# Performance work log

Measured on AMD Instinct MI355X. Metric: run time of the kernel, lower is better.

The kernel has to match this reference:

```python
import jax, jax.numpy as jnp
import numpy as np

B, C, H, W, TF, NH = 16, 512, 24, 24, 512, 8
CPH = C // NH  # channels per head = 64


def setup_inputs() -> dict:
    key = jax.random.key(0)
    ks = jax.random.split(key, 10)
    s = 0.02
    return {
        "x": jax.random.normal(ks[0], (B, C, H, W), jnp.float32),
        "t": jax.random.normal(ks[1], (B, TF), jnp.float32),
        "Wk": jax.random.normal(ks[2], (C, C), jnp.float32) * s,      # 1x1 conv, no bias
        "Wq": jax.random.normal(ks[3], (C, C), jnp.float32) * s,      # 1x1 conv, no bias
        "Wt_w": jax.random.normal(ks[4], (C, TF), jnp.float32) * s,   # Linear weight (out,in)
        "Wt_b": jnp.zeros((C,), jnp.float32),
        "Wm": jax.random.normal(ks[5], (C, C + TF), jnp.float32) * s, # merge 1x1 conv, no bias
        "Wv": jax.random.normal(ks[6], (C, C), jnp.float32) * s,      # 1x1 conv, no bias
        "Wr_w": jax.random.normal(ks[7], (C, C), jnp.float32) * s,    # 1x1 conv with bias
        "Wr_b": jnp.zeros((C,), jnp.float32),
    }


def reference(x, t, Wk, Wq, Wt_w, Wt_b, Wm, Wv, Wr_w, Wr_b):
    b, c, h, w = x.shape
    hw = h * w
    scale = 1.0 / np.sqrt(CPH).astype(np.float32)

    # broadcast text features spatially and merge with image features (1x1 conv)
    t_r = jnp.broadcast_to(t[:, :, None, None], (b, t.shape[1], h, w))
    vl = jnp.einsum('oc,bchw->bohw', Wm, jnp.concatenate([x, t_r], axis=1))
    values = jnp.einsum('oc,bchw->bohw', Wv, vl).reshape(b, NH, CPH, hw)

    # self-attention map: softmax over keys (last dim)
    keys = jnp.einsum('oc,bchw->bohw', Wk, x).reshape(b, NH, CPH, hw)
    queries = jnp.einsum('oc,bchw->bohw', Wq, x).reshape(b, NH, CPH, hw)
    self_att = jax.nn.softmax(
        jnp.einsum('bhcn,bhcm->bhnm', queries, keys) * scale, axis=-1)

    # global cross-attention map: text query vs spatial positions, softmax over hw
    t_m = (t @ Wt_w.T + Wt_b).reshape(b, NH, CPH)
    cross = jax.nn.softmax(
        jnp.einsum('bhcm,bhc->bhm', x.reshape(b, NH, CPH, hw), t_m) * scale, axis=-1)

    # additive combination, then value-weighted aggregation
    att = self_att + cross[:, :, None, :]                    # [b, nh, hw_q, hw_k]
    out = jnp.einsum('bhcm,bhnm->bhcn', values, att).reshape(b, c, h, w)
    out = jnp.einsum('oc,bchw->bohw', Wr_w, out) + Wr_b[None, :, None, None]
    return out
```

## Files before the change

### kernel.cpp

```cpp
#include <hip/hip_runtime.h>
#include <cstdint>
#include <cstddef>

#define NB    16
#define NC    512
#define NHW   576
#define NTF   512
#define NHEAD 8
#define NCPH  64
#define ATT_SCALE 0.125f
#define SCALE_L2E 0.18033688011112042f

typedef float  floatx4 __attribute__((ext_vector_type(4)));
typedef short  short8  __attribute__((ext_vector_type(8)));
typedef unsigned short ushortx4 __attribute__((ext_vector_type(4)));

__device__ __forceinline__ unsigned short f2bf(float f) {
    unsigned int u = __float_as_uint(f);
    u += 0x7fffu + ((u >> 16) & 1u);
    return (unsigned short)(u >> 16);
}
__device__ __forceinline__ float bf2f(unsigned short h) {
    return __uint_as_float(((unsigned int)h) << 16);
}


__global__ void k_prep_weights(const float* __restrict__ Wq, const float* __restrict__ Wk,
                               const float* __restrict__ Wv, const float* __restrict__ Wr,
                               unsigned short* __restrict__ Wqkm,
                               unsigned short* __restrict__ Wv_bf,
                               unsigned short* __restrict__ Wr_bf) {
    int i = blockIdx.x * 256 + threadIdx.x;
    if (i < 1024 * 512) {
        int r = i >> 9, c = i & 511;
        float v = (r < 512) ? Wq[r * 512 + c] : Wk[(r - 512) * 512 + c];
        Wqkm[i] = f2bf(v);
    } else {
        int j = i - 1024 * 512;
        if (j < 512 * 512) Wv_bf[j] = f2bf(Wv[j]);
        else               Wr_bf[j - 512 * 512] = f2bf(Wr[j - 512 * 512]);
    }
}

__global__ void k_prep_wmT(const float* __restrict__ Wm, unsigned short* __restrict__ WmT) {
    __shared__ float tile[32][33];
    int n0 = blockIdx.x * 32, k0 = blockIdx.y * 32;
    int tx = threadIdx.x, ty = threadIdx.y;
    #pragma unroll
    for (int k = 0; k < 4; k++)
        tile[ty + k * 8][tx] = Wm[(size_t)(k0 + ty + k * 8) * 1024 + n0 + tx];
    __syncthreads();
    #pragma unroll
    for (int k = 0; k < 4; k++)
        WmT[(size_t)(n0 + ty + k * 8) * 512 + k0 + tx] = f2bf(tile[tx][ty + k * 8]);
}

__global__ void k_prep_xT(const float* __restrict__ x, unsigned short* __restrict__ xT) {
    __shared__ float tile[32][33];
    int b  = blockIdx.z;
    int p0 = blockIdx.x * 32, c0 = blockIdx.y * 32;
    int tx = threadIdx.x, ty = threadIdx.y;
    const float* xb = x + (size_t)b * NC * NHW;
    #pragma unroll
    for (int k = 0; k < 4; k++)
        tile[ty + k * 8][tx] = xb[(size_t)(c0 + ty + k * 8) * NHW + p0 + tx];
    __syncthreads();
    unsigned short* xTb = xT + (size_t)b * NHW * NC;
    #pragma unroll
    for (int k = 0; k < 4; k++)
        xTb[(size_t)(p0 + ty + k * 8) * NC + c0 + tx] = f2bf(tile[tx][ty + k * 8]);
}

__global__ void k_prep_t(const float* __restrict__ t, const float* __restrict__ Wt_w,
                         const float* __restrict__ Wt_b, const float* __restrict__ Wvm_txt,
                         float* __restrict__ tm, float* __restrict__ tmerge) {
    __shared__ float ts[512];
    int b = blockIdx.x;
    int tid = threadIdx.x;
    ts[tid]       = t[b * 512 + tid];
    ts[tid + 256] = t[b * 512 + tid + 256];
    __syncthreads();
    int oo = blockIdx.y * 256 + tid;
    const float* Wrow = (oo < 512) ? (Wt_w + (size_t)oo * 512)
                                   : (Wvm_txt + (size_t)(oo - 512) * 512);
    float acc = 0.f;
    #pragma unroll 4
    for (int c = 0; c < 512; c += 4) {
        float4 w = *reinterpret_cast<const float4*>(Wrow + c);
        acc += w.x * ts[c] + w.y * ts[c + 1] + w.z * ts[c + 2] + w.w * ts[c + 3];
    }
    if (oo < 512) tm[b * 512 + oo] = acc + Wt_b[oo];
    else          tmerge[b * 512 + (oo - 512)] = acc;
}


__device__ __forceinline__ void g128_stage(const unsigned short* __restrict__ src,
                                           unsigned short* lds, int tid) {
    int row  = tid >> 3;
    int slot = (tid & 7) ^ (row & 7);
    #pragma unroll
    for (int i = 0; i < 4; i++) {
        __builtin_amdgcn_global_load_lds(
            (const __attribute__((address_space(1))) unsigned int*)(src + (size_t)(32 * i + row) * NC + slot * 8),
            (__attribute__((address_space(3))) unsigned int*)(lds + i * 2048 + tid * 8), 16, 0, 0);
    }
}

__device__ __forceinline__ void g128_main(const unsigned short* __restrict__ Asrc,
                                          const unsigned short* __restrict__ Bsrc,
                                          unsigned short (*At)[8192], unsigned short (*Bt)[8192],
                                          int tid, int lane, int wr, int wc,
                                          floatx4 (&acc)[4][4]) {
    int cl = lane & 15, hi = lane >> 4, sx = cl & 7;

    g128_stage(Asrc, At[0], tid);
    g128_stage(Bsrc, Bt[0], tid);
    __syncthreads();

    int buf = 0;
    for (int ks = 0; ks < 8; ks++) {
        if (ks < 7) {
            g128_stage(Asrc + (ks + 1) * 64, At[buf ^ 1], tid);
            g128_stage(Bsrc + (ks + 1) * 64, Bt[buf ^ 1], tid);
        }
        #pragma unroll
        for (int kk = 0; kk < 2; kk++) {
            int sl = ((kk << 2) + hi) ^ sx;
            short8 a[4], bb[4];
            #pragma unroll
            for (int i = 0; i < 4; i++)
                a[i] = *reinterpret_cast<const short8*>(&At[buf][(wr * 64 + i * 16 + cl) * 64 + sl * 8]);
            #pragma unroll
            for (int j = 0; j < 4; j++)
                bb[j] = *reinterpret_cast<const short8*>(&Bt[buf][(wc * 64 + j * 16 + cl) * 64 + sl * 8]);
            #pragma unroll
            for (int i = 0; i < 4; i++)
                #pragma unroll
                for (int j = 0; j < 4; j++)
                    acc[i][j] = __builtin_amdgcn_mfma_f32_16x16x32_bf16(a[i], bb[j], acc[i][j], 0, 0, 0);
        }
        __syncthreads();
        buf ^= 1;
    }
}

__global__ void k_fold(const unsigned short* __restrict__ Wv_bf,
                       const unsigned short* __restrict__ WmT,
                       unsigned short* __restrict__ Wqkm,
                       float* __restrict__ Wvm_txt) {
    __shared__ unsigned short At[2][8192], Bt[2][8192];
    int tid = threadIdx.x, lane = tid & 63, wid = tid >> 6;
    int wr = wid >> 1, wc = wid & 1;
    int m = blockIdx.x >> 3, nt = blockIdx.x & 7;
    int o0 = m * 128, n0 = nt * 128;

    floatx4 acc[4][4];
    floatx4 zz = {0.f, 0.f, 0.f, 0.f};
    #pragma unroll
    for (int i = 0; i < 4; i++)
        #pragma unroll
        for (int j = 0; j < 4; j++) acc[i][j] = zz;

    g128_main(Wv_bf + (size_t)o0 * NC, WmT + (size_t)n0 * NC, At, Bt, tid, lane, wr, wc, acc);

    int cl = lane & 15, r0 = (lane >> 4) * 4;
    #pragma unroll
    for (int i = 0; i < 4; i++)
        #pragma unroll
        for (int jn = 0; jn < 4; jn++) {
            int n = n0 + wc * 64 + jn * 16 + cl;
            #pragma unroll
            for (int j = 0; j < 4; j++) {
                int o = o0 + wr * 64 + i * 16 + r0 + j;
                if (n0 < 512) Wqkm[(size_t)(1024 + o) * 512 + n] = f2bf(acc[i][jn][j]);
                else          Wvm_txt[(size_t)o * 512 + (n - 512)] = acc[i][jn][j];
            }
        }
}

__global__ void k_gemm_qkm(const unsigned short* __restrict__ Wqkm,
                           const unsigned short* __restrict__ xT,
                           const float* __restrict__ tmerge,
                           unsigned short* __restrict__ QT,
                           unsigned short* __restrict__ KT,
                           unsigned short* __restrict__ V) {
    __shared__ unsigned short At[2][8192], Bt[2][8192];
    int tid = threadIdx.x, lane = tid & 63, wid = tid >> 6;
    int wr = wid >> 1, wc = wid & 1;
    int bid = blockIdx.x;
    int xcd = bid & 7, slot = bid >> 3;
    int m = slot / 9, nl = slot % 9;
    int n0 = (xcd * 9 + nl) * 128;
    int o0 = m * 128;

    floatx4 acc[4][4];
    floatx4 zz = {0.f, 0.f, 0.f, 0.f};
    #pragma unroll
    for (int i = 0; i < 4; i++)
        #pragma unroll
        for (int j = 0; j < 4; j++) acc[i][j] = zz;

    g128_main(Wqkm + (size_t)o0 * NC, xT + (size_t)n0 * NC, At, Bt, tid, lane, wr, wc, acc);

    int cl = lane & 15, r0 = (lane >> 4) * 4;
    int ob = (m & 3) * 128 + wr * 64;

    if (m < 8) {
        unsigned short* Yt = (m < 4) ? QT : KT;
        #pragma unroll
        for (int i = 0; i < 4; i++) {
            int ol = ob + i * 16 + r0;
            #pragma unroll
            for (int jn = 0; jn < 4; jn++) {
                int n = n0 + wc * 64 + jn * 16 + cl;
                ushortx4 pk;
                pk[0] = f2bf(acc[i][jn][0]);
                pk[1] = f2bf(acc[i][jn][1]);
                pk[2] = f2bf(acc[i][jn][2]);
                pk[3] = f2bf(acc[i][jn][3]);
                *reinterpret_cast<ushortx4*>(Yt + (size_t)n * NC + ol) = pk;
            }
        }
    } else {
        #pragma unroll
        for (int i = 0; i < 4; i++) {
            int ol = ob + i * 16 + r0;
            #pragma unroll
            for (int jn = 0; jn < 4; jn++) {
                int n = n0 + wc * 64 + jn * 16 + cl;
                int b = n / NHW, p = n - b * NHW;
                float4 tv = *reinterpret_cast<const float4*>(tmerge + b * NC + ol);
                float bias[4] = {tv.x, tv.y, tv.z, tv.w};
                #pragma unroll
                for (int j = 0; j < 4; j++)
                    V[((size_t)b * NC + ol + j) * NHW + p] = f2bf(acc[i][jn][j] + bias[j]);
            }
        }
    }
}

__global__ void k_gemm_final(const unsigned short* __restrict__ Wr_bf,
                             const unsigned short* __restrict__ AO,
                             const float* __restrict__ Wr_b,
                             float* __restrict__ out) {
    __shared__ unsigned short At[2][8192], Bt[2][8192];
    int tid = threadIdx.x, lane = tid & 63, wid = tid >> 6;
    int wr = wid >> 1, wc = wid & 1;
    int bid = blockIdx.x;
    int xcd = bid & 7, slot = bid >> 3;
    int m = slot / 9, nl = slot % 9;
    int n0 = (xcd * 9 + nl) * 128;
    int o0 = m * 128;

    floatx4 acc[4][4];
    floatx4 zz = {0.f, 0.f, 0.f, 0.f};
    #pragma unroll
    for (int i = 0; i < 4; i++)
        #pragma unroll
        for (int j = 0; j < 4; j++) acc[i][j] = zz;

    g128_main(Wr_bf + (size_t)o0 * NC, AO + (size_t)n0 * NC, At, Bt, tid, lane, wr, wc, acc);

    int cl = lane & 15, r0 = (lane >> 4) * 4;
    #pragma unroll
    for (int i = 0; i < 4; i++) {
        float4 bv = *reinterpret_cast<const float4*>(Wr_b + o0 + wr * 64 + i * 16 + r0);
        float bias[4] = {bv.x, bv.y, bv.z, bv.w};
        #pragma unroll
        for (int jn = 0; jn < 4; jn++) {
            int n = n0 + wc * 64 + jn * 16 + cl;
            int b = n / NHW, p = n - b * NHW;
            #pragma unroll
            for (int j = 0; j < 4; j++) {
                int c = o0 + wr * 64 + i * 16 + r0 + j;
                out[((size_t)b * NC + c) * NHW + p] = acc[i][jn][j] + bias[j];
            }
        }
    }
}


__global__ void k_cross_o2(const unsigned short* __restrict__ xT,
                           const unsigned short* __restrict__ V,
                           const float* __restrict__ tm,
                           float* __restrict__ o2) {
    __shared__ float tms[64];
    __shared__ float ss[576];
    __shared__ float red[8];
    __shared__ float part[4][64];
    int bh = blockIdx.x;
    int b = bh >> 3, h = bh & 7;
    int tid = threadIdx.x;

    if (tid < 64) tms[tid] = tm[b * 512 + h * 64 + tid];
    __syncthreads();

    for (int m = tid; m < 576; m += 256) {
        const short8* xr8 = reinterpret_cast<const short8*>(xT + ((size_t)b * NHW + m) * NC + h * 64);
        float acc = 0.f;
        #pragma unroll
        for (int cc = 0; cc < 8; cc++) {
            short8 v8 = xr8[cc];
            #pragma unroll
            for (int q = 0; q < 8; q++)
                acc += bf2f((unsigned short)v8[q]) * tms[cc * 8 + q];
        }
        ss[m] = acc * ATT_SCALE;
    }
    __syncthreads();

    float pmax = -3e38f;
    for (int m = tid; m < 576; m += 256) pmax = fmaxf(pmax, ss[m]);
    #pragma unroll
    for (int off = 32; off; off >>= 1) pmax = fmaxf(pmax, __shfl_xor(pmax, off));
    if ((tid & 63) == 0) red[tid >> 6] = pmax;
    __syncthreads();
    float mx = fmaxf(fmaxf(red[0], red[1]), fmaxf(red[2], red[3]));

    float psum = 0.f;
    for (int m = tid; m < 576; m += 256) {
        float e = __expf(ss[m] - mx);
        ss[m] = e;
        psum += e;
    }
    #pragma unroll
    for (int off = 32; off; off >>= 1) psum += __shfl_xor(psum, off);
    if ((tid & 63) == 0) red[4 + (tid >> 6)] = psum;
    __syncthreads();
    float inv = 1.f / (red[4] + red[5] + red[6] + red[7]);

    int c = tid & 63, seg = tid >> 6;
    const unsigned short* vr = V + ((size_t)b * NC + h * 64 + c) * NHW;
    float pa = 0.f;
    for (int m = seg * 144; m < seg * 144 + 144; m++) pa += bf2f(vr[m]) * ss[m];
    part[seg][c] = pa;
    __syncthreads();
    if (tid < 64)
        o2[(b * 8 + h) * 64 + tid] =
            (part[0][tid] + part[1][tid] + part[2][tid] + part[3][tid]) * inv;
}


__global__ void k_attn(const unsigned short* __restrict__ QT,
                       const unsigned short* __restrict__ KT,
                       const unsigned short* __restrict__ V,
                       const float* __restrict__ o2,
                       unsigned short* __restrict__ AO) {
    __shared__ unsigned short Ktile[2][64][64];
    __shared__ unsigned short Vtile[2][64][64];
    __shared__ unsigned short pbuf[4][16][88];
    int tid  = threadIdx.x;
    int lane = tid & 63, wid = tid >> 6;

    int bid  = blockIdx.x;
    int xcd  = bid & 7;
    int slot = bid >> 3;
    int bh   = xcd * 16 + slot / 9;
    int qt   = slot % 9;
    int b = bh >> 3, h = bh & 7;
    int n0 = qt * 64 + wid * 16;
    int cl = lane & 15;
    int r0 = (lane >> 4) * 4;
    int part = lane >> 4;
    int ko = part * 8;

    const unsigned short* Qb = QT + ((size_t)b * NHW + n0) * NC + h * 64;
    const unsigned short* Kb = KT + (size_t)b * NHW * NC + h * 64;
    const unsigned short* Vb = V  + ((size_t)b * NC + h * 64) * NHW;

    short8 aq0 = *reinterpret_cast<const short8*>(Qb + (size_t)cl * NC + ko);
    short8 aq1 = *reinterpret_cast<const short8*>(Qb + (size_t)cl * NC + 32 + ko);

    int srow = lane >> 3;
    int scol = (lane & 7) ^ srow;

    floatx4 zz = {0.f, 0.f, 0.f, 0.f};
    floatx4 oacc[4] = {zz, zz, zz, zz};
    float es[4] = {0.f, 0.f, 0.f, 0.f};

    {
        const unsigned short* ks = Kb + (size_t)(wid * 16 + srow) * NC + scol * 8;
        const unsigned short* vs = Vb + (size_t)(wid * 16 + srow) * NHW + scol * 8;
        #pragma unroll
        for (int i = 0; i < 2; i++) {
            __builtin_amdgcn_global_load_lds(
                (const __attribute__((address_space(1))) unsigned int*)(ks + (size_t)i * 8 * NC),
                (__attribute__((address_space(3))) unsigned int*)&Ktile[0][wid * 16 + i * 8][0], 16, 0, 0);
            __builtin_amdgcn_global_load_lds(
                (const __attribute__((address_space(1))) unsigned int*)(vs + (size_t)i * 8 * NHW),
                (__attribute__((address_space(3))) unsigned int*)&Vtile[0][wid * 16 + i * 8][0], 16, 0, 0);
        }
    }
    __syncthreads();

    int buf = 0;
    for (int chk = 0; chk < 9; chk++) {
        int m0 = chk * 64;
        if (chk < 8) {
            const unsigned short* ks = Kb + (size_t)(m0 + 64 + wid * 16 + srow) * NC + scol * 8;
            const unsigned short* vs = Vb + (size_t)(wid * 16 + srow) * NHW + (m0 + 64) + scol * 8;
            #pragma unroll
            for (int i = 0; i < 2; i++) {
                __builtin_amdgcn_global_load_lds(
                    (const __attribute__((address_space(1))) unsigned int*)(ks + (size_t)i * 8 * NC),
                    (__attribute__((address_space(3))) unsigned int*)&Ktile[buf ^ 1][wid * 16 + i * 8][0], 16, 0, 0);
                __builtin_amdgcn_global_load_lds(
                    (const __attribute__((address_space(1))) unsigned int*)(vs + (size_t)i * 8 * NHW),
                    (__attribute__((address_space(3))) unsigned int*)&Vtile[buf ^ 1][wid * 16 + i * 8][0], 16, 0, 0);
            }
        }

        floatx4 s[4];
        #pragma unroll
        for (int t = 0; t < 4; t++) {
            int row = t * 16 + cl;
            int sw = cl & 7;
            short8 bk0 = *reinterpret_cast<const short8*>(&Ktile[buf][row][(part ^ sw) * 8]);
            short8 bk1 = *reinterpret_cast<const short8*>(&Ktile[buf][row][((part + 4) ^ sw) * 8]);
            s[t] = __builtin_amdgcn_mfma_f32_16x16x32_bf16(aq0, bk0, zz, 0, 0, 0);
            s[t] = __builtin_amdgcn_mfma_f32_16x16x32_bf16(aq1, bk1, s[t], 0, 0, 0);
        }
        #pragma unroll
        for (int t = 0; t < 4; t++)
            #pragma unroll
            for (int j = 0; j < 4; j++) {
                float e = exp2f(s[t][j] * SCALE_L2E);
                es[j] += e;
                pbuf[wid][r0 + j][t * 16 + cl] = f2bf(e);
            }
        short8 pa0 = *reinterpret_cast<const short8*>(&pbuf[wid][cl][ko]);
        short8 pa1 = *reinterpret_cast<const short8*>(&pbuf[wid][cl][32 + ko]);
        #pragma unroll
        for (int ct = 0; ct < 4; ct++) {
            int row = ct * 16 + cl;
            int sw = cl & 7;
            short8 bv0 = *reinterpret_cast<const short8*>(&Vtile[buf][row][(part ^ sw) * 8]);
            short8 bv1 = *reinterpret_cast<const short8*>(&Vtile[buf][row][((part + 4) ^ sw) * 8]);
            oacc[ct] = __builtin_amdgcn_mfma_f32_16x16x32_bf16(pa0, bv0, oacc[ct], 0, 0, 0);
            oacc[ct] = __builtin_amdgcn_mfma_f32_16x16x32_bf16(pa1, bv1, oacc[ct], 0, 0, 0);
        }
        __syncthreads();
        buf ^= 1;
    }

    #pragma unroll
    for (int off = 1; off < 16; off <<= 1)
        #pragma unroll
        for (int j = 0; j < 4; j++) es[j] += __shfl_xor(es[j], off);
    float ri[4];
    #pragma unroll
    for (int j = 0; j < 4; j++) ri[j] = 1.f / es[j];

    const float* o2b = o2 + bh * 64;
    #pragma unroll
    for (int ct = 0; ct < 4; ct++) {
        float o2v = o2b[ct * 16 + cl];
        #pragma unroll
        for (int j = 0; j < 4; j++)
            pbuf[wid][r0 + j][ct * 16 + cl] = f2bf(oacc[ct][j] * ri[j] + o2v);
    }
    short8 w0 = *reinterpret_cast<const short8*>(&pbuf[wid][cl][part * 16]);
    short8 w1 = *reinterpret_cast<const short8*>(&pbuf[wid][cl][part * 16 + 8]);
    unsigned short* dst = AO + ((size_t)b * NHW + n0 + cl) * NC + h * 64 + part * 16;
    *reinterpret_cast<short8*>(dst)     = w0;
    *reinterpret_cast<short8*>(dst + 8) = w1;
}


extern "C" void kernel_launch(void* const* d_in, const int* in_sizes, int n_in,
                              void* d_out, int out_size, void* d_ws, size_t ws_size,
                              hipStream_t stream) {
    const float* x    = (const float*)d_in[0];
    const float* t    = (const float*)d_in[1];
    const float* Wk   = (const float*)d_in[2];
    const float* Wq   = (const float*)d_in[3];
    const float* Wt_w = (const float*)d_in[4];
    const float* Wt_b = (const float*)d_in[5];
    const float* Wm   = (const float*)d_in[6];
    const float* Wv   = (const float*)d_in[7];
    const float* Wr_w = (const float*)d_in[8];
    const float* Wr_b = (const float*)d_in[9];
    float* out = (float*)d_out;
    char* ws = (char*)d_ws;

    unsigned short* xT      = (unsigned short*)(ws);
    unsigned short* Wqkm    = (unsigned short*)(ws + 9437184);
    unsigned short* Wv_bf   = (unsigned short*)(ws + 11010048);
    unsigned short* Wr_bf   = (unsigned short*)(ws + 11534336);
    float*          tm      = (float*)(ws + 12058624);
    float*          tmerge  = (float*)(ws + 12091392);
    unsigned short* QT      = (unsigned short*)(ws + 12124160);
    unsigned short* KT      = (unsigned short*)(ws + 21561344);
    unsigned short* WmT     = (unsigned short*)(ws + 30998528);
    float*          Wvm_txt = (float*)(ws + 32047104);
    unsigned short* Vv      = (unsigned short*)(ws + 40435712);
    float*          o2      = (float*)(ws + 49872896);
    unsigned short* AO      = xT;
    (void)in_sizes; (void)n_in; (void)out_size; (void)ws_size;

    k_prep_weights<<<4096, 256, 0, stream>>>(Wq, Wk, Wv, Wr_w, Wqkm, Wv_bf, Wr_bf);
    k_prep_wmT<<<dim3(32, 16), dim3(32, 8), 0, stream>>>(Wm, WmT);
    k_prep_xT<<<dim3(18, 16, 16), dim3(32, 8), 0, stream>>>(x, xT);
    k_fold<<<32, 256, 0, stream>>>(Wv_bf, WmT, Wqkm, Wvm_txt);
    k_prep_t<<<dim3(16, 4), 256, 0, stream>>>(t, Wt_w, Wt_b, Wvm_txt, tm, tmerge);
    k_gemm_qkm<<<864, 256, 0, stream>>>(Wqkm, xT, tmerge, QT, KT, Vv);
    k_cross_o2<<<128, 256, 0, stream>>>(xT, Vv, tm, o2);
    k_attn<<<1152, 256, 0, stream>>>(QT, KT, Vv, o2, AO);
    k_gemm_final<<<288, 256, 0, stream>>>(Wr_bf, AO, Wr_b, out);
}
```

Baseline: 124.4 us.

## Merge prep kernels and compute text merge term as matvecs instead of folded matrix

```diff
diff --git a/kernel.cpp b/kernel.cpp
--- a/kernel.cpp
+++ b/kernel.cpp
@@ -24,42 +24,50 @@
     return __uint_as_float(((unsigned int)h) << 16);
 }
 
-
-__global__ void k_prep_weights(const float* __restrict__ Wq, const float* __restrict__ Wk,
-                               const float* __restrict__ Wv, const float* __restrict__ Wr,
-                               unsigned short* __restrict__ Wqkm,
-                               unsigned short* __restrict__ Wv_bf,
-                               unsigned short* __restrict__ Wr_bf) {
-    int i = blockIdx.x * 256 + threadIdx.x;
-    if (i < 1024 * 512) {
-        int r = i >> 9, c = i & 511;
-        float v = (r < 512) ? Wq[r * 512 + c] : Wk[(r - 512) * 512 + c];
-        Wqkm[i] = f2bf(v);
-    } else {
-        int j = i - 1024 * 512;
-        if (j < 512 * 512) Wv_bf[j] = f2bf(Wv[j]);
-        else               Wr_bf[j - 512 * 512] = f2bf(Wr[j - 512 * 512]);
-    }
-}
-
-__global__ void k_prep_wmT(const float* __restrict__ Wm, unsigned short* __restrict__ WmT) {
+__global__ void k_prep_all(const float* __restrict__ Wq, const float* __restrict__ Wk,
+                           const float* __restrict__ Wv, const float* __restrict__ Wr,
+                           const float* __restrict__ Wm, const float* __restrict__ x,
+                           unsigned short* __restrict__ Wqkm,
+                           unsigned short* __restrict__ Wv_bf,
+                           unsigned short* __restrict__ Wr_bf,
+                           unsigned short* __restrict__ WmT,
+                           unsigned short* __restrict__ xT) {
     __shared__ float tile[32][33];
-    int n0 = blockIdx.x * 32, k0 = blockIdx.y * 32;
-    int tx = threadIdx.x, ty = threadIdx.y;
-    #pragma unroll
-    for (int k = 0; k < 4; k++)
-        tile[ty + k * 8][tx] = Wm[(size_t)(k0 + ty + k * 8) * 1024 + n0 + tx];
-    __syncthreads();
-    #pragma unroll
-    for (int k = 0; k < 4; k++)
-        WmT[(size_t)(n0 + ty + k * 8) * 512 + k0 + tx] = f2bf(tile[tx][ty + k * 8]);
-}
-
-__global__ void k_prep_xT(const float* __restrict__ x, unsigned short* __restrict__ xT) {
-    __shared__ float tile[32][33];
-    int b  = blockIdx.z;
-    int p0 = blockIdx.x * 32, c0 = blockIdx.y * 32;
-    int tx = threadIdx.x, ty = threadIdx.y;
+    int bid = blockIdx.x;
+    int tid = threadIdx.x;
+
+    if (bid < 4096) {
+        int i = bid * 256 + tid;
+        if (i < 1024 * 512) {
+            int r = i >> 9, c = i & 511;
+            float v = (r < 512) ? Wq[r * 512 + c] : Wk[(r - 512) * 512 + c];
+            Wqkm[i] = f2bf(v);
+        } else {
+            int j = i - 1024 * 512;
+            if (j < 512 * 512) Wv_bf[j] = f2bf(Wv[j]);
+            else               Wr_bf[j - 512 * 512] = f2bf(Wr[j - 512 * 512]);
+        }
+        return;
+    }
+
+    int tx = tid & 31, ty = tid >> 5;
+    if (bid < 4352) {
+        int bi = bid - 4096;
+        int n0 = (bi & 15) * 32, k0 = (bi >> 4) * 32;
+        #pragma unroll
+        for (int k = 0; k < 4; k++)
+            tile[ty + k * 8][tx] = Wm[(size_t)(k0 + ty + k * 8) * 1024 + n0 + tx];
+        __syncthreads();
+        #pragma unroll
+        for (int k = 0; k < 4; k++)
+            WmT[(size_t)(n0 + ty + k * 8) * 512 + k0 + tx] = f2bf(tile[tx][ty + k * 8]);
+        return;
+    }
+
+    int bi = bid - 4352;
+    int pi = bi % 18, rem = bi / 18;
+    int ci = rem & 15, b = rem >> 4;
+    int p0 = pi * 32, c0 = ci * 32;
     const float* xb = x + (size_t)b * NC * NHW;
     #pragma unroll
     for (int k = 0; k < 4; k++)
@@ -72,25 +80,50 @@
 }
 
 __global__ void k_prep_t(const float* __restrict__ t, const float* __restrict__ Wt_w,
-                         const float* __restrict__ Wt_b, const float* __restrict__ Wvm_txt,
+                         const float* __restrict__ Wt_b, const float* __restrict__ Wm,
+                         const float* __restrict__ Wv,
                          float* __restrict__ tm, float* __restrict__ tmerge) {
     __shared__ float ts[512];
-    int b = blockIdx.x;
-    int tid = threadIdx.x;
+    __shared__ float us[512];
+    int b = blockIdx.x, tid = threadIdx.x;
     ts[tid]       = t[b * 512 + tid];
     ts[tid + 256] = t[b * 512 + tid + 256];
     __syncthreads();
-    int oo = blockIdx.y * 256 + tid;
-    const float* Wrow = (oo < 512) ? (Wt_w + (size_t)oo * 512)
-                                   : (Wvm_txt + (size_t)(oo - 512) * 512);
-    float acc = 0.f;
-    #pragma unroll 4
-    for (int c = 0; c < 512; c += 4) {
-        float4 w = *reinterpret_cast<const float4*>(Wrow + c);
-        acc += w.x * ts[c] + w.y * ts[c + 1] + w.z * ts[c + 2] + w.w * ts[c + 3];
-    }
-    if (oo < 512) tm[b * 512 + oo] = acc + Wt_b[oo];
-    else          tmerge[b * 512 + (oo - 512)] = acc;
+
+    if (blockIdx.y == 0) {
+        for (int oo = tid; oo < 512; oo += 256) {
+            const float* Wrow = Wt_w + (size_t)oo * 512;
+            float acc = 0.f;
+            #pragma unroll 4
+            for (int c = 0; c < 512; c += 4) {
+                float4 w = *reinterpret_cast<const float4*>(Wrow + c);
+                acc += w.x * ts[c] + w.y * ts[c + 1] + w.z * ts[c + 2] + w.w * ts[c + 3];
+            }
+            tm[b * 512 + oo] = acc + Wt_b[oo];
+        }
+    } else {
+        for (int c = tid; c < 512; c += 256) {
+            const float* Wrow = Wm + (size_t)c * 1024 + 512;
+            float acc = 0.f;
+            #pragma unroll 4
+            for (int j = 0; j < 512; j += 4) {
+                float4 w = *reinterpret_cast<const float4*>(Wrow + j);
+                acc += w.x * ts[j] + w.y * ts[j + 1] + w.z * ts[j + 2] + w.w * ts[j + 3];
+            }
+            us[c] = acc;
+        }
+        __syncthreads();
+        for (int oo = tid; oo < 512; oo += 256) {
+            const float* Wrow = Wv + (size_t)oo * 512;
+            float acc = 0.f;
+            #pragma unroll 4
+            for (int c = 0; c < 512; c += 4) {
+                float4 w = *reinterpret_cast<const float4*>(Wrow + c);
+                acc += w.x * us[c] + w.y * us[c + 1] + w.z * us[c + 2] + w.w * us[c + 3];
+            }
+            tmerge[b * 512 + oo] = acc;
+        }
+    }
 }
 
 
@@ -146,12 +179,11 @@
 
 __global__ void k_fold(const unsigned short* __restrict__ Wv_bf,
                        const unsigned short* __restrict__ WmT,
-                       unsigned short* __restrict__ Wqkm,
-                       float* __restrict__ Wvm_txt) {
+                       unsigned short* __restrict__ Wqkm) {
     __shared__ unsigned short At[2][8192], Bt[2][8192];
     int tid = threadIdx.x, lane = tid & 63, wid = tid >> 6;
     int wr = wid >> 1, wc = wid & 1;
-    int m = blockIdx.x >> 3, nt = blockIdx.x & 7;
+    int m = blockIdx.x >> 2, nt = blockIdx.x & 3;
     int o0 = m * 128, n0 = nt * 128;
 
     floatx4 acc[4][4];
@@ -172,8 +204,7 @@
             #pragma unroll
             for (int j = 0; j < 4; j++) {
                 int o = o0 + wr * 64 + i * 16 + r0 + j;
-                if (n0 < 512) Wqkm[(size_t)(1024 + o) * 512 + n] = f2bf(acc[i][jn][j]);
-                else          Wvm_txt[(size_t)o * 512 + (n - 512)] = acc[i][jn][j];
+                Wqkm[(size_t)(1024 + o) * 512 + n] = f2bf(acc[i][jn][j]);
             }
         }
 }
@@ -492,17 +523,14 @@
     unsigned short* QT      = (unsigned short*)(ws + 12124160);
     unsigned short* KT      = (unsigned short*)(ws + 21561344);
     unsigned short* WmT     = (unsigned short*)(ws + 30998528);
-    float*          Wvm_txt = (float*)(ws + 32047104);
     unsigned short* Vv      = (unsigned short*)(ws + 40435712);
     float*          o2      = (float*)(ws + 49872896);
     unsigned short* AO      = xT;
     (void)in_sizes; (void)n_in; (void)out_size; (void)ws_size;
 
-    k_prep_weights<<<4096, 256, 0, stream>>>(Wq, Wk, Wv, Wr_w, Wqkm, Wv_bf, Wr_bf);
-    k_prep_wmT<<<dim3(32, 16), dim3(32, 8), 0, stream>>>(Wm, WmT);
-    k_prep_xT<<<dim3(18, 16, 16), dim3(32, 8), 0, stream>>>(x, xT);
-    k_fold<<<32, 256, 0, stream>>>(Wv_bf, WmT, Wqkm, Wvm_txt);
-    k_prep_t<<<dim3(16, 4), 256, 0, stream>>>(t, Wt_w, Wt_b, Wvm_txt, tm, tmerge);
+    k_prep_all<<<8960, 256, 0, stream>>>(Wq, Wk, Wv, Wr_w, Wm, x, Wqkm, Wv_bf, Wr_bf, WmT, xT);
+    k_fold<<<16, 256, 0, stream>>>(Wv_bf, WmT, Wqkm);
+    k_prep_t<<<dim3(16, 2), 256, 0, stream>>>(t, Wt_w, Wt_b, Wm, Wv, tm, tmerge);
     k_gemm_qkm<<<864, 256, 0, stream>>>(Wqkm, xT, tmerge, QT, KT, Vv);
     k_cross_o2<<<128, 256, 0, stream>>>(xT, Vv, tm, o2);
     k_attn<<<1152, 256, 0, stream>>>(QT, KT, Vv, o2, AO);
```

New measurement: 160.2 us. 28.8% more time.
